# Kernel optimization log

Hardware: AMD Instinct MI355X
Metric: run time of the kernel (lower is better)

## Reference

```python
import jax, jax.numpy as jnp
import numpy as np

N_NODES = 100000
N_EDGES = 1600000
N_FEAT = 128
HIDDEN = 64
NUM_GRAPHS = 64


def setup_inputs() -> dict:
    key = jax.random.key(0)
    ks = jax.random.split(key, 10)
    x = jax.random.normal(ks[0], (N_NODES, N_FEAT), dtype=jnp.float32)
    W = jax.random.normal(ks[1], (N_FEAT, HIDDEN), dtype=jnp.float32) * (1.0 / np.sqrt(N_FEAT))
    b = jax.random.normal(ks[2], (HIDDEN,), dtype=jnp.float32) * 0.01
    W1 = jax.random.normal(ks[3], (HIDDEN, 16), dtype=jnp.float32) * (1.0 / np.sqrt(HIDDEN))
    b1 = jax.random.normal(ks[4], (16,), dtype=jnp.float32) * 0.01
    W2 = jax.random.normal(ks[5], (16, 1), dtype=jnp.float32) * 0.25
    b2 = jax.random.normal(ks[6], (1,), dtype=jnp.float32) * 0.01
    edge_index = jax.random.randint(ks[7], (2, N_EDGES), 0, N_NODES, dtype=jnp.int64)
    batch = jnp.sort(jax.random.randint(ks[8], (N_NODES,), 0, NUM_GRAPHS, dtype=jnp.int64))
    return {"x": x, "W": W, "b": b, "W1": W1, "b1": b1, "W2": W2, "b2": b2,
            "edge_index": edge_index, "batch": batch, "num_graphs": NUM_GRAPHS}


def reference(x, W, b, W1, b1, W2, b2, edge_index, batch, num_graphs):
    N = x.shape[0]
    # GCNConv: h = D^-1/2 (A + I) D^-1/2 (x W) + b
    h = x @ W  # [N, H]
    loops = jnp.arange(N, dtype=edge_index.dtype)
    src = jnp.concatenate([edge_index[0], loops])  # source nodes (with self-loops)
    dst = jnp.concatenate([edge_index[1], loops])  # target nodes
    deg = jax.ops.segment_sum(jnp.ones(dst.shape, h.dtype), dst, num_segments=N)
    dis = jnp.where(deg > 0, jax.lax.rsqrt(deg), 0.0)  # deg^-1/2, 0 for isolated
    norm = dis[src] * dis[dst]  # [E+N]
    msg = h[src] * norm[:, None]  # gather + normalize
    agg = jax.ops.segment_sum(msg, dst, num_segments=N) + b  # scatter-add + bias
    hn = jax.nn.relu(agg)
    # global_add_pool over graphs
    u = jax.ops.segment_sum(hn, batch, num_segments=num_graphs)  # [G, H]
    out = jax.nn.relu(u @ W1 + b1) @ W2 + b2  # [G, 1]
    return out.reshape(-1)
```

## Files before the change

kernel.cpp:

```cpp
#include <hip/hip_runtime.h>

#define N_NODES   100000
#define N_FEAT    128
#define N_EDGES   1600000
#define HIDDEN    64
#define NUM_GRAPHS 64
#define CHUNK   4096
#define NCHUNK  ((N_EDGES + CHUNK - 1) / CHUNK)
#define BSHIFT  8
#define NBUCKET ((N_NODES + 255) >> 8)
#define OFFS_W  (NBUCKET + 1)
#define CAP     4800
#define QE      ((CAP + 511) / 512)
#define WT_BLOCKS 4
#define GEMM_GRID ((N_NODES + 127) / 128)

typedef unsigned int  uint32;
typedef unsigned short ushort16;

typedef __attribute__((ext_vector_type(8))) __bf16 bf16x8;
typedef __attribute__((ext_vector_type(4))) float  f32x4;
union Frag8 { bf16x8 v; unsigned short s[8]; uint4 q; };

static __device__ __forceinline__ unsigned short f2bf(float f) {
    uint32 u = __float_as_uint(f);
    u += 0x7fffu + ((u >> 16) & 1u);
    return (unsigned short)(u >> 16);
}

__global__ __launch_bounds__(512) void k_pre(const float* __restrict__ W,
                                             ushort16* __restrict__ Wt,
                                             const int* __restrict__ ei,
                                             int* __restrict__ src_out,
                                             unsigned char* __restrict__ dst8,
                                             int* __restrict__ offs) {
    __shared__ int hist[512];
    __shared__ int excl[512];
    __shared__ int ssrc[CHUNK];
    __shared__ int sdst[CHUNK];

    if (blockIdx.x < WT_BLOCKS) {
        const int base = blockIdx.x * 2048 + threadIdx.x;
#pragma unroll
        for (int j = 0; j < 4; ++j) {
            const int idx = base + j * 512;
            const int k = idx >> 6, n = idx & 63;
            Wt[n * N_FEAT + k] = f2bf(W[idx]);
        }
        return;
    }

    const int c = blockIdx.x - WT_BLOCKS;
    const int base = c * CHUNK;
    const int n = min(CHUNK, N_EDGES - base);
    const int t = threadIdx.x;
    hist[t] = 0;
    __syncthreads();

    int es[CHUNK / 512], ed[CHUNK / 512], rk[CHUNK / 512];
#pragma unroll
    for (int k = 0; k < CHUNK / 512; ++k) {
        const int i = t + k * 512;
        if (i < n) {
            ed[k] = __builtin_nontemporal_load(&ei[N_EDGES + base + i]);
            es[k] = __builtin_nontemporal_load(&ei[base + i]);
            rk[k] = atomicAdd(&hist[ed[k] >> BSHIFT], 1);
        }
    }
    __syncthreads();

    const int cnt = hist[t];
    for (int off = 1; off < 512; off <<= 1) {
        const int v = (t >= off) ? hist[t - off] : 0;
        __syncthreads();
        hist[t] += v;
        __syncthreads();
    }
    excl[t] = hist[t] - cnt;
    __syncthreads();
    if (t <= NBUCKET) offs[c * OFFS_W + t] = base + excl[t];

#pragma unroll
    for (int k = 0; k < CHUNK / 512; ++k) {
        const int i = t + k * 512;
        if (i < n) {
            const int pos = excl[ed[k] >> BSHIFT] + rk[k];
            ssrc[pos] = es[k];
            sdst[pos] = ed[k];
        }
    }
    __syncthreads();

    for (int i = t; i < n; i += 512)
        src_out[base + i] = ssrc[i];
    for (int i = t * 4; i < n; i += 2048) {
        const uint32 p = (uint32)(sdst[i] & 255)
                       | ((uint32)(sdst[i + 1] & 255) << 8)
                       | ((uint32)(sdst[i + 2] & 255) << 16)
                       | ((uint32)(sdst[i + 3] & 255) << 24);
        *(uint32*)&dst8[base + i] = p;
    }
}

__global__ __launch_bounds__(512) void k_mix(const float* __restrict__ x,
                                             const ushort16* __restrict__ Wt,
                                             ushort16* __restrict__ hb,
                                             const int* __restrict__ offs,
                                             const int* __restrict__ src_tmp,
                                             const unsigned char* __restrict__ dst8,
                                             int* __restrict__ srcs,
                                             int* __restrict__ row_ptr,
                                             int* __restrict__ row_end,
                                             float* __restrict__ dis) {
    __shared__ int hist[256];
    __shared__ int nxt[256];
    __shared__ int segb[NCHUNK];
    __shared__ int pre[NCHUNK + 1];
    __shared__ int sc[512];
    __shared__ int ssrc[CAP];
    __shared__ int sb;

    if (blockIdx.x >= NBUCKET) {
        const int t    = threadIdx.x;
        const int lane = t & 63;
        const int wv   = t >> 6;
        const int m15  = lane & 15;
        const int quad = lane >> 4;
        const int base = (blockIdx.x - NBUCKET) * 128 + wv * 16;
        const int arow = min(base + m15, N_NODES - 1);

        const float* xr = &x[(size_t)arow * N_FEAT + quad * 8];
        float4 xa[4][2];
#pragma unroll
        for (int kc = 0; kc < 4; ++kc) {
            xa[kc][0] = *(const float4*)&xr[kc * 32];
            xa[kc][1] = *(const float4*)&xr[kc * 32 + 4];
        }

        Frag8 bfr[4][4];
#pragma unroll
        for (int nt = 0; nt < 4; ++nt) {
            const ushort16* wr = &Wt[(nt * 16 + m15) * N_FEAT + quad * 8];
#pragma unroll
            for (int kc = 0; kc < 4; ++kc)
                bfr[nt][kc].q = *(const uint4*)&wr[kc * 32];
        }

        Frag8 af[4];
#pragma unroll
        for (int kc = 0; kc < 4; ++kc) {
            const float* f = (const float*)&xa[kc][0];
#pragma unroll
            for (int j = 0; j < 8; ++j) af[kc].s[j] = f2bf(f[j]);
        }

        f32x4 acc[4];
#pragma unroll
        for (int nt = 0; nt < 4; ++nt) acc[nt] = (f32x4){0.f, 0.f, 0.f, 0.f};

#pragma unroll
        for (int kc = 0; kc < 4; ++kc)
#pragma unroll
            for (int nt = 0; nt < 4; ++nt)
                acc[nt] = __builtin_amdgcn_mfma_f32_16x16x32_bf16(af[kc].v, bfr[nt][kc].v,
                                                                  acc[nt], 0, 0, 0);

#pragma unroll
        for (int r = 0; r < 4; ++r) {
            const int orow = base + quad * 4 + r;
            if (orow < N_NODES) {
#pragma unroll
                for (int nt = 0; nt < 4; ++nt)
                    hb[(size_t)orow * HIDDEN + nt * 16 + m15] = f2bf(acc[nt][r]);
            }
        }
        return;
    }

    const int b = blockIdx.x;
    const int lo = b << BSHIFT;
    const int t = threadIdx.x;

    if (t < 256) hist[t] = 0;
    if (t == 0) sb = 0;
    __syncthreads();

    int len = 0;
    if (t < NCHUNK) {
        const int s0 = offs[t * OFFS_W + b];
        const int s1 = offs[t * OFFS_W + b + 1];
        segb[t] = s0;
        len = s1 - s0;
        atomicAdd(&sb, s0 - t * CHUNK);
    }
    sc[t] = len;
    __syncthreads();
    for (int off = 1; off < 512; off <<= 1) {
        const int v = (t >= off) ? sc[t - off] : 0;
        __syncthreads();
        sc[t] += v;
        __syncthreads();
    }
    if (t == 0) pre[0] = 0;
    if (t < NCHUNK) pre[t + 1] = sc[t];
    __syncthreads();

    const int total  = pre[NCHUNK];
    const int bstart = sb;
    const bool fits  = (total <= CAP);

    int es[QE], ed[QE], rk[QE];
    int ne = 0;
    if (fits) {
        for (int e = t; e < total; e += 512) {
            int l2 = 0, h2 = NCHUNK;
            while (h2 - l2 > 1) { const int mid = (l2 + h2) >> 1;
                                  if (pre[mid] <= e) l2 = mid; else h2 = mid; }
            const int gidx = segb[l2] + (e - pre[l2]);
            const int d = dst8[gidx];
            const int s = src_tmp[gidx];
            es[ne] = s; ed[ne] = d;
            rk[ne] = atomicAdd(&hist[d], 1);
            ++ne;
        }
    } else {
        const int lane = t & 63, wv = t >> 6;
        for (int c = wv; c < NCHUNK; c += 8)
            for (int i = segb[c] + lane; i < segb[c] + (pre[c + 1] - pre[c]); i += 64)
                atomicAdd(&hist[dst8[i]], 1);
    }
    __syncthreads();

    const int cnt = (t < 256) ? hist[t] : 0;
    for (int off = 1; off < 256; off <<= 1) {
        int v = 0;
        if (t < 256 && t >= off) v = hist[t - off];
        __syncthreads();
        if (t < 256) hist[t] += v;
        __syncthreads();
    }
    if (t < 256) {
        const int excl = hist[t] - cnt;
        nxt[t] = excl;
        const int node = lo + t;
        if (node < N_NODES) {
            row_ptr[node] = bstart + excl;
            row_end[node] = bstart + excl + cnt;
            dis[node]     = rsqrtf((float)cnt + 1.0f);
        }
    }
    __syncthreads();

    if (fits) {
        for (int k = 0; k < ne; ++k)
            ssrc[nxt[ed[k]] + rk[k]] = es[k];
        __syncthreads();
        for (int i = t; i < total; i += 512)
            srcs[bstart + i] = ssrc[i];
    } else {
        const int lane = t & 63, wv = t >> 6;
        for (int c = wv; c < NCHUNK; c += 8)
            for (int i = segb[c] + lane; i < segb[c] + (pre[c + 1] - pre[c]); i += 64) {
                const int d = dst8[i];
                const int pos = atomicAdd(&nxt[d], 1);
                srcs[bstart + pos] = src_tmp[i];
            }
    }
}

__global__ __launch_bounds__(512) void k_agg(const int* __restrict__ rp_g,
                                             const int* __restrict__ re_g,
                                             const int* __restrict__ srcs,
                                             const ushort16* __restrict__ hb,
                                             const float* __restrict__ dis,
                                             const float* __restrict__ bias,
                                             const int* __restrict__ batch,
                                             float* __restrict__ u) {
    __shared__ float sp[128 * 65];
    __shared__ int   rp[256];
    __shared__ int   rc[256];
    __shared__ float sdn[256];
    __shared__ int   gbs[256];
    const int b  = blockIdx.x;
    const int lo = b << BSHIFT;
    const int t  = threadIdx.x;

    if (t < 256) {
        const int node = lo + t;
        const bool ok = node < N_NODES;
        const int p = ok ? rp_g[node] : 0;
        rp[t]  = p;
        rc[t]  = ok ? (re_g[node] - p) : 0;
        sdn[t] = ok ? dis[node] : 0.f;
        gbs[t] = ok ? batch[node] : 0;
    }
    __syncthreads();

    const int lane = t & 63;
    const int k    = lane & 7;
    const int kb   = lane & 56;
    const int grp  = (t >> 6) * 8 + (lane >> 3);

    float acc[4][8];
#pragma unroll
    for (int a = 0; a < 4; ++a)
#pragma unroll
        for (int j = 0; j < 8; ++j) acc[a][j] = 0.f;

#pragma unroll
    for (int a = 0; a < 4; ++a) {
        const int n   = grp * 4 + a;
        const int beg = rp[n];
        const int L   = rc[n];
        for (int i = 0; i < L; i += 8) {
            const int idx = beg + min(i + k, L - 1);
            const int sv  = srcs[idx];
            const float wv_ = dis[sv];
            uint4 v[8];
            float w[8];
#pragma unroll
            for (int j = 0; j < 8; ++j) {
                const int sj = __shfl(sv, kb | j);
                w[j] = __shfl(wv_, kb | j);
                v[j] = *(const uint4*)&hb[(size_t)sj * HIDDEN + k * 8];
            }
            const int rem = L - i;
#pragma unroll
            for (int j = 0; j < 8; ++j) {
                const float m = (j < rem) ? w[j] : 0.f;
                acc[a][0] = fmaf(__uint_as_float(v[j].x << 16),         m, acc[a][0]);
                acc[a][1] = fmaf(__uint_as_float(v[j].x & 0xffff0000u), m, acc[a][1]);
                acc[a][2] = fmaf(__uint_as_float(v[j].y << 16),         m, acc[a][2]);
                acc[a][3] = fmaf(__uint_as_float(v[j].y & 0xffff0000u), m, acc[a][3]);
                acc[a][4] = fmaf(__uint_as_float(v[j].z << 16),         m, acc[a][4]);
                acc[a][5] = fmaf(__uint_as_float(v[j].z & 0xffff0000u), m, acc[a][5]);
                acc[a][6] = fmaf(__uint_as_float(v[j].w << 16),         m, acc[a][6]);
                acc[a][7] = fmaf(__uint_as_float(v[j].w & 0xffff0000u), m, acc[a][7]);
            }
        }
    }

    const float4 b0 = *(const float4*)&bias[k * 8];
    const float4 b1 = *(const float4*)&bias[k * 8 + 4];
    const int f   = t & 63;
    const int seg = t >> 6;

    for (int h = 0; h < 2; ++h) {
        if ((grp >> 5) == h) {
#pragma unroll
            for (int a = 0; a < 4; ++a) {
                const int n = grp * 4 + a;
                const int nl = n - h * 128;
                const uint4 hv = *(const uint4*)
                    &hb[(size_t)min(lo + n, N_NODES - 1) * HIDDEN + k * 8];
                const float dn = sdn[n];
                float4 r0, r1;
                r0.x = fmaxf(fmaf(fmaf(__uint_as_float(hv.x << 16),         dn, acc[a][0]), dn, b0.x), 0.f);
                r0.y = fmaxf(fmaf(fmaf(__uint_as_float(hv.x & 0xffff0000u), dn, acc[a][1]), dn, b0.y), 0.f);
                r0.z = fmaxf(fmaf(fmaf(__uint_as_float(hv.y << 16),         dn, acc[a][2]), dn, b0.z), 0.f);
                r0.w = fmaxf(fmaf(fmaf(__uint_as_float(hv.y & 0xffff0000u), dn, acc[a][3]), dn, b0.w), 0.f);
                r1.x = fmaxf(fmaf(fmaf(__uint_as_float(hv.z << 16),         dn, acc[a][4]), dn, b1.x), 0.f);
                r1.y = fmaxf(fmaf(fmaf(__uint_as_float(hv.z & 0xffff0000u), dn, acc[a][5]), dn, b1.y), 0.f);
                r1.z = fmaxf(fmaf(fmaf(__uint_as_float(hv.w << 16),         dn, acc[a][6]), dn, b1.z), 0.f);
                r1.w = fmaxf(fmaf(fmaf(__uint_as_float(hv.w & 0xffff0000u), dn, acc[a][7]), dn, b1.w), 0.f);
                *(float4*)&sp[nl * 65 + k * 8]     = r0;
                *(float4*)&sp[nl * 65 + k * 8 + 4] = r1;
            }
        }
        __syncthreads();

        float a_ = 0.f;
        int   cg = -1;
        for (int n2 = seg * 16; n2 < seg * 16 + 16; ++n2) {
            const int node = lo + h * 128 + n2;
            if (node >= N_NODES) break;
            const float r = sp[n2 * 65 + f];
            const int gr = gbs[h * 128 + n2];
            if (gr != cg) {
                if (cg >= 0) atomicAdd(&u[cg * HIDDEN + f], a_);
                cg = gr; a_ = r;
            } else {
                a_ += r;
            }
        }
        if (cg >= 0) atomicAdd(&u[cg * HIDDEN + f], a_);
        __syncthreads();
    }
}

__global__ __launch_bounds__(64) void mlp_kernel(const float* __restrict__ u,
                                                 const float* __restrict__ W1,
                                                 const float* __restrict__ b1,
                                                 const float* __restrict__ W2,
                                                 const float* __restrict__ b2,
                                                 float* __restrict__ out) {
    __shared__ float W1s[HIDDEN * 16];
    __shared__ float W2s[16];
    __shared__ float b1s[16];
    const int t = threadIdx.x;
    for (int i = t; i < HIDDEN * 16; i += 64) W1s[i] = W1[i];
    if (t < 16) { W2s[t] = W2[t]; b1s[t] = b1[t]; }
    __syncthreads();
    if (t < NUM_GRAPHS) {
        float uu[HIDDEN];
#pragma unroll
        for (int k = 0; k < HIDDEN; ++k) uu[k] = u[t * HIDDEN + k];
        float o = b2[0];
#pragma unroll
        for (int j = 0; j < 16; ++j) {
            float s = b1s[j];
#pragma unroll
            for (int k = 0; k < HIDDEN; ++k) s = fmaf(uu[k], W1s[k * 16 + j], s);
            o = fmaf(fmaxf(s, 0.f), W2s[j], o);
        }
        out[t] = o;
    }
}

extern "C" void kernel_launch(void* const* d_in, const int* in_sizes, int n_in,
                              void* d_out, int out_size, void* d_ws, size_t ws_size,
                              hipStream_t stream) {
    const float* x  = (const float*)d_in[0];
    const float* W  = (const float*)d_in[1];
    const float* b  = (const float*)d_in[2];
    const float* W1 = (const float*)d_in[3];
    const float* b1 = (const float*)d_in[4];
    const float* W2 = (const float*)d_in[5];
    const float* b2 = (const float*)d_in[6];
    const int*   ei = (const int*)d_in[7];
    const int* batch = (const int*)d_in[8];
    float* out = (float*)d_out;

    ushort16* hb       = (ushort16*)d_ws;
    int*      src_tmp  = (int*)(hb + (size_t)N_NODES * HIDDEN);
    unsigned char* dst8 = (unsigned char*)(src_tmp + N_EDGES);
    int*      srcs     = (int*)(dst8 + N_EDGES);
    int*      offs     = srcs + N_EDGES;
    int*      row_ptr  = offs + NCHUNK * OFFS_W;
    int*      row_end  = row_ptr + N_NODES;
    float*    dis      = (float*)(row_end + N_NODES);
    float*    u        = dis + N_NODES;
    ushort16* Wtg      = (ushort16*)(u + NUM_GRAPHS * HIDDEN);

    hipMemsetAsync(u, 0, NUM_GRAPHS * HIDDEN * sizeof(float), stream);

    k_pre<<<WT_BLOCKS + NCHUNK, 512, 0, stream>>>(W, Wtg, ei, src_tmp, dst8, offs);
    k_mix<<<NBUCKET + GEMM_GRID, 512, 0, stream>>>(x, Wtg, hb, offs, src_tmp, dst8,
                                                   srcs, row_ptr, row_end, dis);
    k_agg<<<NBUCKET, 512, 0, stream>>>(row_ptr, row_end, srcs, hb, dis, b, batch, u);
    mlp_kernel<<<1, 64, 0, stream>>>(u, W1, b1, W2, b2, out);
}
```

Measured before the change: 191.7 us.

## Use wave-shuffle scans, chunk map lookup, and smaller aggregation blocks

Replaces the shared-memory Hillis-Steele scans in k_pre and k_mix with wavefront shuffle scans that need only two barriers. Swaps the per-edge binary search over chunk prefixes for a shared chunk-index map filled by each chunk thread. Shrinks the aggregation kernel to 256 threads covering 64 nodes per block, giving about 1563 blocks instead of 391 so load balances better and the two-pass pool loop goes away. The cost is more blocks doing atomics into u and extra shared memory for the chunk map.

```diff
diff --git a/kernel.cpp b/kernel.cpp
--- a/kernel.cpp
+++ b/kernel.cpp
@@ -14,6 +14,8 @@
 #define QE      ((CAP + 511) / 512)
 #define WT_BLOCKS 4
 #define GEMM_GRID ((N_NODES + 127) / 128)
+#define AGG_NODES 64
+#define AGG_BLOCKS ((N_NODES + AGG_NODES - 1) / AGG_NODES)
 
 typedef unsigned int  uint32;
 typedef unsigned short ushort16;
@@ -26,6 +28,54 @@
     uint32 u = __float_as_uint(f);
     u += 0x7fffu + ((u >> 16) & 1u);
     return (unsigned short)(u >> 16);
+}
+
+static __device__ __forceinline__ int scan512(int v, int t, int* wsum) {
+    const int lane = t & 63;
+    const int wv   = t >> 6;
+#pragma unroll
+    for (int off = 1; off < 64; off <<= 1) {
+        const int n = __shfl_up(v, off);
+        if (lane >= off) v += n;
+    }
+    if (lane == 63) wsum[wv] = v;
+    __syncthreads();
+    if (t < 8) {
+        int s = wsum[t];
+#pragma unroll
+        for (int off = 1; off < 8; off <<= 1) {
+            const int n = __shfl_up(s, off);
+            if (t >= off) s += n;
+        }
+        wsum[t] = s;
+    }
+    __syncthreads();
+    if (wv > 0) v += wsum[wv - 1];
+    return v;
+}
+
+static __device__ __forceinline__ int scan256(int v, int t, int* wsum) {
+    const int lane = t & 63;
+    const int wv   = t >> 6;
+#pragma unroll
+    for (int off = 1; off < 64; off <<= 1) {
+        const int n = __shfl_up(v, off);
+        if (lane >= off) v += n;
+    }
+    if (lane == 63 && wv < 4) wsum[wv] = v;
+    __syncthreads();
+    if (t < 4) {
+        int s = wsum[t];
+#pragma unroll
+        for (int off = 1; off < 4; off <<= 1) {
+            const int n = __shfl_up(s, off);
+            if (t >= off) s += n;
+        }
+        wsum[t] = s;
+    }
+    __syncthreads();
+    if (wv > 0 && wv < 4) v += wsum[wv - 1];
+    return v;
 }
 
 __global__ __launch_bounds__(512) void k_pre(const float* __restrict__ W,
@@ -36,6 +86,7 @@
                                              int* __restrict__ offs) {
     __shared__ int hist[512];
     __shared__ int excl[512];
+    __shared__ int wsum[8];
     __shared__ int ssrc[CHUNK];
     __shared__ int sdst[CHUNK];
 
@@ -70,13 +121,8 @@
     __syncthreads();
 
     const int cnt = hist[t];
-    for (int off = 1; off < 512; off <<= 1) {
-        const int v = (t >= off) ? hist[t - off] : 0;
-        __syncthreads();
-        hist[t] += v;
-        __syncthreads();
-    }
-    excl[t] = hist[t] - cnt;
+    const int inc = scan512(cnt, t, wsum);
+    excl[t] = inc - cnt;
     __syncthreads();
     if (t <= NBUCKET) offs[c * OFFS_W + t] = base + excl[t];
 
@@ -116,8 +162,9 @@
     __shared__ int nxt[256];
     __shared__ int segb[NCHUNK];
     __shared__ int pre[NCHUNK + 1];
-    __shared__ int sc[512];
+    __shared__ unsigned short cmap[CAP];
     __shared__ int ssrc[CAP];
+    __shared__ int wsum[8];
     __shared__ int sb;
 
     if (blockIdx.x >= NBUCKET) {
@@ -193,16 +240,9 @@
         len = s1 - s0;
         atomicAdd(&sb, s0 - t * CHUNK);
     }
-    sc[t] = len;
-    __syncthreads();
-    for (int off = 1; off < 512; off <<= 1) {
-        const int v = (t >= off) ? sc[t - off] : 0;
-        __syncthreads();
-        sc[t] += v;
-        __syncthreads();
-    }
+    const int inc = scan512(len, t, wsum);
     if (t == 0) pre[0] = 0;
-    if (t < NCHUNK) pre[t + 1] = sc[t];
+    if (t < NCHUNK) pre[t + 1] = inc;
     __syncthreads();
 
     const int total  = pre[NCHUNK];
@@ -210,57 +250,56 @@
     const bool fits  = (total <= CAP);
 
     int es[QE], ed[QE], rk[QE];
-    int ne = 0;
     if (fits) {
-        for (int e = t; e < total; e += 512) {
-            int l2 = 0, h2 = NCHUNK;
-            while (h2 - l2 > 1) { const int mid = (l2 + h2) >> 1;
-                                  if (pre[mid] <= e) l2 = mid; else h2 = mid; }
-            const int gidx = segb[l2] + (e - pre[l2]);
-            const int d = dst8[gidx];
-            const int s = src_tmp[gidx];
-            es[ne] = s; ed[ne] = d;
-            rk[ne] = atomicAdd(&hist[d], 1);
-            ++ne;
+        if (t < NCHUNK) {
+            const int p0 = pre[t], p1 = pre[t + 1];
+            for (int j = p0; j < p1; ++j) cmap[j] = (unsigned short)t;
+        }
+        __syncthreads();
+#pragma unroll
+        for (int q = 0; q < QE; ++q) {
+            const int e = t + q * 512;
+            if (e < total) {
+                const int c2 = cmap[e];
+                const int gidx = segb[c2] + (e - pre[c2]);
+                ed[q] = dst8[gidx];
+                es[q] = src_tmp[gidx];
+                rk[q] = atomicAdd(&hist[ed[q]], 1);
+            }
         }
     } else {
         const int lane = t & 63, wv = t >> 6;
-        for (int c = wv; c < NCHUNK; c += 8)
-            for (int i = segb[c] + lane; i < segb[c] + (pre[c + 1] - pre[c]); i += 64)
+        for (int c2 = wv; c2 < NCHUNK; c2 += 8)
+            for (int i = segb[c2] + lane; i < segb[c2] + (pre[c2 + 1] - pre[c2]); i += 64)
                 atomicAdd(&hist[dst8[i]], 1);
     }
     __syncthreads();
 
-    const int cnt = (t < 256) ? hist[t] : 0;
-    for (int off = 1; off < 256; off <<= 1) {
-        int v = 0;
-        if (t < 256 && t >= off) v = hist[t - off];
-        __syncthreads();
-        if (t < 256) hist[t] += v;
-        __syncthreads();
-    }
+    const int cv  = (t < 256) ? hist[t] : 0;
+    const int hin = scan256(cv, t, wsum);
     if (t < 256) {
-        const int excl = hist[t] - cnt;
+        const int excl = hin - cv;
         nxt[t] = excl;
         const int node = lo + t;
         if (node < N_NODES) {
             row_ptr[node] = bstart + excl;
-            row_end[node] = bstart + excl + cnt;
-            dis[node]     = rsqrtf((float)cnt + 1.0f);
+            row_end[node] = bstart + excl + cv;
+            dis[node]     = rsqrtf((float)cv + 1.0f);
         }
     }
     __syncthreads();
 
     if (fits) {
-        for (int k = 0; k < ne; ++k)
-            ssrc[nxt[ed[k]] + rk[k]] = es[k];
+#pragma unroll
+        for (int q = 0; q < QE; ++q)
+            if (t + q * 512 < total) ssrc[nxt[ed[q]] + rk[q]] = es[q];
         __syncthreads();
         for (int i = t; i < total; i += 512)
             srcs[bstart + i] = ssrc[i];
     } else {
         const int lane = t & 63, wv = t >> 6;
-        for (int c = wv; c < NCHUNK; c += 8)
-            for (int i = segb[c] + lane; i < segb[c] + (pre[c + 1] - pre[c]); i += 64) {
+        for (int c2 = wv; c2 < NCHUNK; c2 += 8)
+            for (int i = segb[c2] + lane; i < segb[c2] + (pre[c2 + 1] - pre[c2]); i += 64) {
                 const int d = dst8[i];
                 const int pos = atomicAdd(&nxt[d], 1);
                 srcs[bstart + pos] = src_tmp[i];
@@ -268,7 +307,7 @@
     }
 }
 
-__global__ __launch_bounds__(512) void k_agg(const int* __restrict__ rp_g,
+__global__ __launch_bounds__(256) void k_agg(const int* __restrict__ rp_g,
                                              const int* __restrict__ re_g,
                                              const int* __restrict__ srcs,
                                              const ushort16* __restrict__ hb,
@@ -276,16 +315,16 @@
                                              const float* __restrict__ bias,
                                              const int* __restrict__ batch,
                                              float* __restrict__ u) {
-    __shared__ float sp[128 * 65];
-    __shared__ int   rp[256];
-    __shared__ int   rc[256];
-    __shared__ float sdn[256];
-    __shared__ int   gbs[256];
+    __shared__ float sp[AGG_NODES * 65];
+    __shared__ int   rp[AGG_NODES];
+    __shared__ int   rc[AGG_NODES];
+    __shared__ float sdn[AGG_NODES];
+    __shared__ int   gbs[AGG_NODES];
     const int b  = blockIdx.x;
-    const int lo = b << BSHIFT;
+    const int lo = b * AGG_NODES;
     const int t  = threadIdx.x;
 
-    if (t < 256) {
+    if (t < AGG_NODES) {
         const int node = lo + t;
         const bool ok = node < N_NODES;
         const int p = ok ? rp_g[node] : 0;
@@ -301,15 +340,15 @@
     const int kb   = lane & 56;
     const int grp  = (t >> 6) * 8 + (lane >> 3);
 
-    float acc[4][8];
-#pragma unroll
-    for (int a = 0; a < 4; ++a)
+    float acc[2][8];
+#pragma unroll
+    for (int a = 0; a < 2; ++a)
 #pragma unroll
         for (int j = 0; j < 8; ++j) acc[a][j] = 0.f;
 
 #pragma unroll
-    for (int a = 0; a < 4; ++a) {
-        const int n   = grp * 4 + a;
+    for (int a = 0; a < 2; ++a) {
+        const int n   = grp * 2 + a;
         const int beg = rp[n];
         const int L   = rc[n];
         for (int i = 0; i < L; i += 8) {
@@ -342,50 +381,43 @@
 
     const float4 b0 = *(const float4*)&bias[k * 8];
     const float4 b1 = *(const float4*)&bias[k * 8 + 4];
+#pragma unroll
+    for (int a = 0; a < 2; ++a) {
+        const int n = grp * 2 + a;
+        const uint4 hv = *(const uint4*)
+            &hb[(size_t)min(lo + n, N_NODES - 1) * HIDDEN + k * 8];
+        const float dn = sdn[n];
+        float4 r0, r1;
+        r0.x = fmaxf(fmaf(fmaf(__uint_as_float(hv.x << 16),         dn, acc[a][0]), dn, b0.x), 0.f);
+        r0.y = fmaxf(fmaf(fmaf(__uint_as_float(hv.x & 0xffff0000u), dn, acc[a][1]), dn, b0.y), 0.f);
+        r0.z = fmaxf(fmaf(fmaf(__uint_as_float(hv.y << 16),         dn, acc[a][2]), dn, b0.z), 0.f);
+        r0.w = fmaxf(fmaf(fmaf(__uint_as_float(hv.y & 0xffff0000u), dn, acc[a][3]), dn, b0.w), 0.f);
+        r1.x = fmaxf(fmaf(fmaf(__uint_as_float(hv.z << 16),         dn, acc[a][4]), dn, b1.x), 0.f);
+        r1.y = fmaxf(fmaf(fmaf(__uint_as_float(hv.z & 0xffff0000u), dn, acc[a][5]), dn, b1.y), 0.f);
+        r1.z = fmaxf(fmaf(fmaf(__uint_as_float(hv.w << 16),         dn, acc[a][6]), dn, b1.z), 0.f);
+        r1.w = fmaxf(fmaf(fmaf(__uint_as_float(hv.w & 0xffff0000u), dn, acc[a][7]), dn, b1.w), 0.f);
+        *(float4*)&sp[n * 65 + k * 8]     = r0;
+        *(float4*)&sp[n * 65 + k * 8 + 4] = r1;
+    }
+    __syncthreads();
+
     const int f   = t & 63;
     const int seg = t >> 6;
-
-    for (int h = 0; h < 2; ++h) {
-        if ((grp >> 5) == h) {
-#pragma unroll
-            for (int a = 0; a < 4; ++a) {
-                const int n = grp * 4 + a;
-                const int nl = n - h * 128;
-                const uint4 hv = *(const uint4*)
-                    &hb[(size_t)min(lo + n, N_NODES - 1) * HIDDEN + k * 8];
-                const float dn = sdn[n];
-                float4 r0, r1;
-                r0.x = fmaxf(fmaf(fmaf(__uint_as_float(hv.x << 16),         dn, acc[a][0]), dn, b0.x), 0.f);
-                r0.y = fmaxf(fmaf(fmaf(__uint_as_float(hv.x & 0xffff0000u), dn, acc[a][1]), dn, b0.y), 0.f);
-                r0.z = fmaxf(fmaf(fmaf(__uint_as_float(hv.y << 16),         dn, acc[a][2]), dn, b0.z), 0.f);
-                r0.w = fmaxf(fmaf(fmaf(__uint_as_float(hv.y & 0xffff0000u), dn, acc[a][3]), dn, b0.w), 0.f);
-                r1.x = fmaxf(fmaf(fmaf(__uint_as_float(hv.z << 16),         dn, acc[a][4]), dn, b1.x), 0.f);
-                r1.y = fmaxf(fmaf(fmaf(__uint_as_float(hv.z & 0xffff0000u), dn, acc[a][5]), dn, b1.y), 0.f);
-                r1.z = fmaxf(fmaf(fmaf(__uint_as_float(hv.w << 16),         dn, acc[a][6]), dn, b1.z), 0.f);
-                r1.w = fmaxf(fmaf(fmaf(__uint_as_float(hv.w & 0xffff0000u), dn, acc[a][7]), dn, b1.w), 0.f);
-                *(float4*)&sp[nl * 65 + k * 8]     = r0;
-                *(float4*)&sp[nl * 65 + k * 8 + 4] = r1;
-            }
-        }
-        __syncthreads();
-
-        float a_ = 0.f;
-        int   cg = -1;
-        for (int n2 = seg * 16; n2 < seg * 16 + 16; ++n2) {
-            const int node = lo + h * 128 + n2;
-            if (node >= N_NODES) break;
-            const float r = sp[n2 * 65 + f];
-            const int gr = gbs[h * 128 + n2];
-            if (gr != cg) {
-                if (cg >= 0) atomicAdd(&u[cg * HIDDEN + f], a_);
-                cg = gr; a_ = r;
-            } else {
-                a_ += r;
-            }
-        }
-        if (cg >= 0) atomicAdd(&u[cg * HIDDEN + f], a_);
-        __syncthreads();
-    }
+    float a_ = 0.f;
+    int   cg = -1;
+    for (int n2 = seg * 16; n2 < seg * 16 + 16; ++n2) {
+        const int node = lo + n2;
+        if (node >= N_NODES) break;
+        const float r = sp[n2 * 65 + f];
+        const int gr = gbs[n2];
+        if (gr != cg) {
+            if (cg >= 0) atomicAdd(&u[cg * HIDDEN + f], a_);
+            cg = gr; a_ = r;
+        } else {
+            a_ += r;
+        }
+    }
+    if (cg >= 0) atomicAdd(&u[cg * HIDDEN + f], a_);
 }
 
 __global__ __launch_bounds__(64) void mlp_kernel(const float* __restrict__ u,
@@ -447,6 +479,6 @@
     k_pre<<<WT_BLOCKS + NCHUNK, 512, 0, stream>>>(W, Wtg, ei, src_tmp, dst8, offs);
     k_mix<<<NBUCKET + GEMM_GRID, 512, 0, stream>>>(x, Wtg, hb, offs, src_tmp, dst8,
                                                    srcs, row_ptr, row_end, dis);
-    k_agg<<<NBUCKET, 512, 0, stream>>>(row_ptr, row_end, srcs, hb, dis, b, batch, u);
+    k_agg<<<AGG_BLOCKS, 256, 0, stream>>>(row_ptr, row_end, srcs, hb, dis, b, batch, u);
     mlp_kernel<<<1, 64, 0, stream>>>(u, W1, b1, W2, b2, out);
 }
```

After: 177.3 us. 1.08x faster.
